# Kernel optimization log

Hardware: AMD Instinct MI355X
Metric: run time of the kernel (lower is better)

## Reference

```python
import jax, jax.numpy as jnp
import numpy as np

N_E, N_C, H = 100000, 50000, 256
D_E, D_C = 768, 1024
E_EE, E_EC, E_CE = 800000, 400000, 400000
EPS = 1e-12


def setup_inputs() -> dict:
    key = jax.random.key(0)
    ks = jax.random.split(key, 16)
    x_entity = jax.random.normal(ks[0], (N_E, D_E), jnp.float32)
    x_chunk = jax.random.normal(ks[1], (N_C, D_C), jnp.float32)
    # edge[0] = source indices, edge[1] = destination indices
    edge_ee = jnp.stack([jax.random.randint(ks[2], (E_EE,), 0, N_E),
                         jax.random.randint(ks[3], (E_EE,), 0, N_E)])
    edge_ec = jnp.stack([jax.random.randint(ks[4], (E_EC,), 0, N_E),
                         jax.random.randint(ks[5], (E_EC,), 0, N_C)])
    edge_ce = jnp.stack([jax.random.randint(ks[6], (E_CE,), 0, N_C),
                         jax.random.randint(ks[7], (E_CE,), 0, N_E)])
    # per-type projection weights (stored [in, out]; y = x @ W)
    P_e = jax.random.normal(ks[8], (D_E, H), jnp.float32) / np.sqrt(D_E).astype(np.float32)
    P_c = jax.random.normal(ks[9], (D_C, H), jnp.float32) / np.sqrt(D_C).astype(np.float32)
    s = np.float32(1.0 / np.sqrt(H))
    # SAGEConv params stacked over the 3 edge types: 0=e->e, 1=e->c, 2=c->e
    Wl1 = jax.random.normal(ks[10], (3, H, H), jnp.float32) * s
    bl1 = jnp.zeros((3, H), jnp.float32)
    Wr1 = jax.random.normal(ks[11], (3, H, H), jnp.float32) * s
    Wl2 = jax.random.normal(ks[12], (3, H, H), jnp.float32) * s
    bl2 = jnp.zeros((3, H), jnp.float32)
    Wr2 = jax.random.normal(ks[13], (3, H, H), jnp.float32) * s
    return {"x_entity": x_entity, "x_chunk": x_chunk,
            "edge_ee": edge_ee, "edge_ec": edge_ec, "edge_ce": edge_ce,
            "P_e": P_e, "P_c": P_c,
            "Wl1": Wl1, "bl1": bl1, "Wr1": Wr1,
            "Wl2": Wl2, "bl2": bl2, "Wr2": Wr2}


def _sage(x_src, x_dst, edge, Wl, bl, Wr, n_dst):
    # PyG SAGEConv: lin_l(mean of neighbor features) + lin_r(x_dst)
    msg = x_src[edge[0]]                                   # [E, H] gather
    agg = jax.ops.segment_sum(msg, edge[1], num_segments=n_dst)
    cnt = jax.ops.segment_sum(jnp.ones((edge.shape[1], 1), x_src.dtype),
                              edge[1], num_segments=n_dst)
    mean = agg / jnp.maximum(cnt, 1.0)                     # isolated nodes -> 0
    return mean @ Wl + bl + x_dst @ Wr


def _l2norm(v):
    # F.normalize(v, dim=1), eps=1e-12
    n = jnp.sqrt(jnp.sum(v * v, axis=1, keepdims=True))
    return v / jnp.maximum(n, EPS)


def reference(x_entity, x_chunk, edge_ee, edge_ec, edge_ce,
              P_e, P_c, Wl1, bl1, Wr1, Wl2, bl2, Wr2):
    # per-type projection (bias=False)
    h_e = x_entity @ P_e
    h_c = x_chunk @ P_c
    id_e, id_c = h_e, h_c
    # conv1: HeteroConv(aggr='sum') -> sum SAGE outputs per destination type
    o_e = (_sage(h_e, h_e, edge_ee, Wl1[0], bl1[0], Wr1[0], N_E)
           + _sage(h_c, h_e, edge_ce, Wl1[2], bl1[2], Wr1[2], N_E))
    o_c = _sage(h_e, h_c, edge_ec, Wl1[1], bl1[1], Wr1[1], N_C)
    # dropout(0.1) is identity in eval; relu then residual
    h_e = jax.nn.relu(o_e) + id_e
    h_c = jax.nn.relu(o_c) + id_c
    # conv2
    o_e = (_sage(h_e, h_e, edge_ee, Wl2[0], bl2[0], Wr2[0], N_E)
           + _sage(h_c, h_e, edge_ce, Wl2[2], bl2[2], Wr2[2], N_E))
    o_c = _sage(h_e, h_c, edge_ec, Wl2[1], bl2[1], Wr2[1], N_C)
    return _l2norm(o_e), _l2norm(o_c)
```

## Files before the change

kernel.cpp:

```cpp
#include <hip/hip_runtime.h>
#include <hip/hip_bf16.h>

#define N_E 100000
#define N_C 50000
#define H 256
#define D_E 768
#define D_C 1024
#define E_EE 800000
#define E_EC 400000
#define E_CE 400000
#define E_TOT (E_EE + E_CE + E_EC)

#define ME_PAD 100096
#define MC_PAD 50048

#define LDSZ 24576

typedef unsigned short u16;
typedef __attribute__((ext_vector_type(8))) short bf16x8;
typedef __attribute__((ext_vector_type(4))) float f32x4;

__device__ __forceinline__ float bf2f(u16 x) {
    unsigned u = ((unsigned)x) << 16;
    return __builtin_bit_cast(float, u);
}
__device__ __forceinline__ u16 f2bf(float f) {
    unsigned u = __builtin_bit_cast(unsigned, f);
    u = (u + 0x7fffu + ((u >> 16) & 1u)) >> 16;
    return (u16)u;
}

struct TransJobs {
    const float* a[12];
    const float* b[12];
    u16* dst[12];
    int K[12];
};

__global__ __launch_bounds__(1024) void transpose_all_k(TransJobs t) {
    int j = blockIdx.z;
    int K = t.K[j];
    int k0 = blockIdx.x * 32;
    if (k0 >= K) return;
    int n0 = blockIdx.y * 32;
    __shared__ float sm[32][33];
    int tx = threadIdx.x, ty = threadIdx.y;
    size_t idx = (size_t)(k0 + ty) * H + n0 + tx;
    float v = t.a[j][idx];
    if (t.b[j]) v += t.b[j][idx];
    sm[ty][tx] = v;
    __syncthreads();
    t.dst[j][(size_t)(n0 + ty) * K + k0 + tx] = f2bf(sm[tx][ty]);
}

__global__ __launch_bounds__(256) void hist3_k(const int* __restrict__ eeD,
                                               const int* __restrict__ ceD,
                                               const int* __restrict__ ecD,
                                               int* __restrict__ cnt) {
    int i = blockIdx.x * 256 + threadIdx.x;
    if (i >= E_TOT) return;
    if (i < E_EE) atomicAdd(&cnt[eeD[i]], 1);
    else if (i < E_EE + E_CE) atomicAdd(&cnt[N_E + ceD[i - E_EE]], 1);
    else atomicAdd(&cnt[2 * N_E + ecD[i - E_EE - E_CE]], 1);
}

#define SCAN_N (2 * N_E + N_C)
#define SCAN_NB ((SCAN_N + 1023) / 1024)

__global__ __launch_bounds__(1024) void scan_blk_k(const int* __restrict__ cnt,
                                                   int* __restrict__ part,
                                                   int* __restrict__ bsum) {
    __shared__ int sm[1024];
    int i = blockIdx.x * 1024 + threadIdx.x;
    int v = (i < SCAN_N) ? cnt[i] : 0;
    sm[threadIdx.x] = v;
    __syncthreads();
    for (int off = 1; off < 1024; off <<= 1) {
        int t = (threadIdx.x >= off) ? sm[threadIdx.x - off] : 0;
        __syncthreads();
        sm[threadIdx.x] += t;
        __syncthreads();
    }
    if (i < SCAN_N) part[i] = sm[threadIdx.x] - v;
    if (threadIdx.x == 1023) bsum[blockIdx.x] = sm[1023];
}

__global__ __launch_bounds__(1024) void scan_top_k(int* __restrict__ bsum) {
    __shared__ int sm[1024];
    int v = (threadIdx.x < SCAN_NB) ? bsum[threadIdx.x] : 0;
    sm[threadIdx.x] = v;
    __syncthreads();
    for (int off = 1; off < 1024; off <<= 1) {
        int t = (threadIdx.x >= off) ? sm[threadIdx.x - off] : 0;
        __syncthreads();
        sm[threadIdx.x] += t;
        __syncthreads();
    }
    if (threadIdx.x < SCAN_NB) bsum[threadIdx.x] = sm[threadIdx.x] - v;
}

__global__ __launch_bounds__(1024) void scan_out_k(const int* __restrict__ part,
                                                   const int* __restrict__ bsum,
                                                   int* __restrict__ eePtr,
                                                   int* __restrict__ cePtr,
                                                   int* __restrict__ ecPtr,
                                                   int* __restrict__ curAll) {
    int i = blockIdx.x * 1024 + threadIdx.x;
    if (i < SCAN_N) {
        int v = part[i] + bsum[blockIdx.x];
        int w;
        if (i < N_E) {
            w = v; eePtr[i] = w;
        } else if (i < 2 * N_E) {
            w = v - E_EE; cePtr[i - N_E] = w;
        } else {
            w = v - (E_EE + E_CE); ecPtr[i - 2 * N_E] = w;
        }
        curAll[i] = w;
    }
    if (i == 0) {
        eePtr[N_E] = E_EE;
        cePtr[N_E] = E_CE;
        ecPtr[N_C] = E_EC;
    }
}

__global__ __launch_bounds__(256) void reorder3_k(const int* __restrict__ eeS, const int* __restrict__ eeD,
                                                  const int* __restrict__ ceS, const int* __restrict__ ceD,
                                                  const int* __restrict__ ecS, const int* __restrict__ ecD,
                                                  int* __restrict__ curAll, int* __restrict__ srcAll) {
    int i = blockIdx.x * 256 + threadIdx.x;
    if (i >= E_TOT) return;
    if (i < E_EE) {
        int pos = atomicAdd(&curAll[eeD[i]], 1);
        srcAll[pos] = eeS[i];
    } else if (i < E_EE + E_CE) {
        int k = i - E_EE;
        int pos = atomicAdd(&curAll[N_E + ceD[k]], 1);
        srcAll[E_EE + pos] = ceS[k];
    } else {
        int k = i - E_EE - E_CE;
        int pos = atomicAdd(&curAll[2 * N_E + ecD[k]], 1);
        srcAll[E_EE + E_CE + pos] = ecS[k];
    }
}

struct GatherArgs {
    const u16* feat[3];
    const int* rowptr[3];
    const int* srcIdx[3];
    u16* outAgg[3];
    int nDst[3];
    int blkEnd[3];
};

__device__ __forceinline__ void acc8(float* a, uint4 v) {
    a[0] += __builtin_bit_cast(float, v.x << 16);
    a[1] += __builtin_bit_cast(float, v.x & 0xffff0000u);
    a[2] += __builtin_bit_cast(float, v.y << 16);
    a[3] += __builtin_bit_cast(float, v.y & 0xffff0000u);
    a[4] += __builtin_bit_cast(float, v.z << 16);
    a[5] += __builtin_bit_cast(float, v.z & 0xffff0000u);
    a[6] += __builtin_bit_cast(float, v.w << 16);
    a[7] += __builtin_bit_cast(float, v.w & 0xffff0000u);
}

__global__ __launch_bounds__(256) void gather3_k(GatherArgs a) {
    const int b = blockIdx.x;
    const int j = (b >= a.blkEnd[0]) + (b >= a.blkEnd[1]);
    const int b0 = j ? a.blkEnd[j - 1] : 0;
    const int r = (b - b0) * 4 + (threadIdx.x >> 6);
    const int lane = threadIdx.x & 63;
    const int half = lane >> 5;
    const int pos = lane & 31;

    float acc[8] = {};
    int deg = 0;
    if (r < a.nDst[j]) {
        const int* __restrict__ rp = a.rowptr[j];
        const int* __restrict__ si = a.srcIdx[j];
        const u16* __restrict__ ft = a.feat[j];
        int e0 = rp[r], e1 = rp[r + 1];
        deg = e1 - e0;
        int e = e0;
        for (; e + 7 < e1; e += 8) {
            int sA = si[e + half];
            int sB = si[e + 2 + half];
            int sC = si[e + 4 + half];
            int sD = si[e + 6 + half];
            uint4 vA = *(const uint4*)(ft + (size_t)sA * H + pos * 8);
            uint4 vB = *(const uint4*)(ft + (size_t)sB * H + pos * 8);
            uint4 vC = *(const uint4*)(ft + (size_t)sC * H + pos * 8);
            uint4 vD = *(const uint4*)(ft + (size_t)sD * H + pos * 8);
            acc8(acc, vA); acc8(acc, vB); acc8(acc, vC); acc8(acc, vD);
        }
        for (; e + 3 < e1; e += 4) {
            int sA = si[e + half];
            int sB = si[e + 2 + half];
            uint4 vA = *(const uint4*)(ft + (size_t)sA * H + pos * 8);
            uint4 vB = *(const uint4*)(ft + (size_t)sB * H + pos * 8);
            acc8(acc, vA); acc8(acc, vB);
        }
        for (; e + 1 < e1; e += 2) {
            int s = si[e + half];
            uint4 v = *(const uint4*)(ft + (size_t)s * H + pos * 8);
            acc8(acc, v);
        }
        if (e < e1 && half == 0) {
            int s = si[e];
            uint4 v = *(const uint4*)(ft + (size_t)s * H + pos * 8);
            acc8(acc, v);
        }
    }
#pragma unroll
    for (int k = 0; k < 8; ++k) acc[k] += __shfl_xor(acc[k], 32);

    if (half == 0) {
        float inv = deg > 0 ? 1.f / (float)deg : 0.f;
        uint4 o;
        o.x = (unsigned)f2bf(acc[0] * inv) | ((unsigned)f2bf(acc[1] * inv) << 16);
        o.y = (unsigned)f2bf(acc[2] * inv) | ((unsigned)f2bf(acc[3] * inv) << 16);
        o.z = (unsigned)f2bf(acc[4] * inv) | ((unsigned)f2bf(acc[5] * inv) << 16);
        o.w = (unsigned)f2bf(acc[6] * inv) | ((unsigned)f2bf(acc[7] * inv) << 16);
        *(uint4*)(a.outAgg[j] + (size_t)r * H + pos * 8) = o;
    }
}

struct GemmCfg {
    const u16* A[3];
    const u16* Wt[3];
    int nPairs;
    const float* bias1;
    const float* bias2;
    const u16* res;
    void* out;
    int Mvalid;
    int mode;
};
struct ConvArgs2 {
    GemmCfg c[2];
    int blkSplit;
};

__global__ __launch_bounds__(512, 4) void gemm_conv_k(ConvArgs2 gg) {
    const int which = blockIdx.x >= gg.blkSplit;
    const GemmCfg* __restrict__ g = which ? &gg.c[1] : &gg.c[0];
    const int row0 = (blockIdx.x - (which ? gg.blkSplit : 0)) * 128;

    __shared__ char lds[3][LDSZ];
    __shared__ float rowsq[128];
    const int tid = threadIdx.x;
    const int lane = tid & 63;
    const int wid = tid >> 6;
    const int wm = wid >> 2;
    const int wn = wid & 3;

    const int srow = tid >> 2;
    const int au = (tid & 3) ^ ((srow >> 1) & 3);
    const int ofsA = (row0 + srow) * H + au * 8;
    const int ofsB1 = srow * H + au * 8;
    const int brow2 = 128 + srow;
    const int bu2 = (tid & 3) ^ ((brow2 >> 1) & 3);
    const int ofsB2 = brow2 * H + bu2 * 8;

    int a_off[4], b_off[4];
#pragma unroll
    for (int mi = 0; mi < 4; ++mi) {
        int row = wm * 64 + mi * 16 + (lane & 15);
        int u = (lane >> 4) ^ ((row >> 1) & 3);
        a_off[mi] = row * 64 + u * 16;
    }
#pragma unroll
    for (int ni = 0; ni < 4; ++ni) {
        int row = wn * 64 + ni * 16 + (lane & 15);
        int u = (lane >> 4) ^ ((row >> 1) & 3);
        b_off[ni] = 8192 + row * 64 + u * 16;
    }

#define STAGE(p_, kk_, buf_)                                                                      \
    do {                                                                                          \
        const u16* A_ = g->A[p_];                                                                 \
        const u16* W_ = g->Wt[p_];                                                                \
        __builtin_amdgcn_global_load_lds(                                                         \
            (const __attribute__((address_space(1))) void*)(A_ + ofsA + (kk_)),                   \
            (__attribute__((address_space(3))) void*)((buf_) + wid * 1024), 16, 0, 0);            \
        __builtin_amdgcn_global_load_lds(                                                         \
            (const __attribute__((address_space(1))) void*)(W_ + ofsB1 + (kk_)),                  \
            (__attribute__((address_space(3))) void*)((buf_) + 8192 + wid * 1024), 16, 0, 0);     \
        __builtin_amdgcn_global_load_lds(                                                         \
            (const __attribute__((address_space(1))) void*)(W_ + ofsB2 + (kk_)),                  \
            (__attribute__((address_space(3))) void*)((buf_) + 16384 + wid * 1024), 16, 0, 0);    \
    } while (0)

    f32x4 acc[4][4] = {};
    const int T = g->nPairs * (H >> 5);

    char* bufC = lds[0];
    char* bufN = lds[1];
    char* bufS = lds[2];

    STAGE(0, 0, bufC);
    STAGE(0, 32, bufN);
    int pn = 0, kn = 64;
    if (kn == H) { kn = 0; pn = 1; }

    for (int s = 0; s < T; ++s) {
        if (s + 2 < T) {
            STAGE(pn, kn, bufS);
            kn += 32;
            if (kn == H) { kn = 0; ++pn; }
            asm volatile("s_waitcnt vmcnt(6)" ::: "memory");
        } else if (s + 1 < T) {
            asm volatile("s_waitcnt vmcnt(3)" ::: "memory");
        } else {
            asm volatile("s_waitcnt vmcnt(0)" ::: "memory");
        }
        __builtin_amdgcn_sched_barrier(0);
        __builtin_amdgcn_s_barrier();

        bf16x8 af[4], bfr[4];
#pragma unroll
        for (int mi = 0; mi < 4; ++mi)
            af[mi] = *reinterpret_cast<const bf16x8*>(bufC + a_off[mi]);
#pragma unroll
        for (int ni = 0; ni < 4; ++ni)
            bfr[ni] = *reinterpret_cast<const bf16x8*>(bufC + b_off[ni]);
#pragma unroll
        for (int mi = 0; mi < 4; ++mi)
#pragma unroll
            for (int ni = 0; ni < 4; ++ni)
                acc[mi][ni] = __builtin_amdgcn_mfma_f32_16x16x32_bf16(af[mi], bfr[ni],
                                                                      acc[mi][ni], 0, 0, 0);
        __builtin_amdgcn_sched_barrier(0);
        __builtin_amdgcn_s_barrier();
        char* t = bufC; bufC = bufN; bufN = bufS; bufS = t;
    }
#undef STAGE

    const int ccol = wn * 64 + (lane & 15);
    const int crow0 = row0 + wm * 64 + ((lane >> 4) << 2);
    float bv[4];
#pragma unroll
    for (int ni = 0; ni < 4; ++ni) {
        int c = ccol + ni * 16;
        float b = 0.f;
        if (g->bias1) b += g->bias1[c];
        if (g->bias2) b += g->bias2[c];
        bv[ni] = b;
    }

    if (g->mode == 1) {
#pragma unroll
        for (int ni = 0; ni < 4; ++ni) {
            int c = ccol + ni * 16;
#pragma unroll
            for (int mi = 0; mi < 4; ++mi) {
#pragma unroll
                for (int j = 0; j < 4; ++j) {
                    int r = crow0 + mi * 16 + j;
                    size_t idx = (size_t)r * H + c;
                    float v = fmaxf(acc[mi][ni][j] + bv[ni], 0.f) + bf2f(g->res[idx]);
                    ((u16*)g->out)[idx] = f2bf(v);
                }
            }
        }
    } else {
        if (tid < 128) rowsq[tid] = 0.f;
        __syncthreads();
#pragma unroll
        for (int mi = 0; mi < 4; ++mi) {
#pragma unroll
            for (int j = 0; j < 4; ++j) {
                float p = 0.f;
#pragma unroll
                for (int ni = 0; ni < 4; ++ni) {
                    float v = acc[mi][ni][j] + bv[ni];
                    p += v * v;
                }
                p += __shfl_xor(p, 1);
                p += __shfl_xor(p, 2);
                p += __shfl_xor(p, 4);
                p += __shfl_xor(p, 8);
                if ((lane & 15) == 0) {
                    int rl = wm * 64 + mi * 16 + ((lane >> 4) << 2) + j;
                    atomicAdd(&rowsq[rl], p);
                }
            }
        }
        __syncthreads();
#pragma unroll
        for (int mi = 0; mi < 4; ++mi) {
#pragma unroll
            for (int j = 0; j < 4; ++j) {
                int rl = wm * 64 + mi * 16 + ((lane >> 4) << 2) + j;
                int r = row0 + rl;
                if (r < g->Mvalid) {
                    float inv = 1.f / fmaxf(sqrtf(rowsq[rl]), 1e-12f);
#pragma unroll
                    for (int ni = 0; ni < 4; ++ni) {
                        int c = ccol + ni * 16;
                        float v = acc[mi][ni][j] + bv[ni];
                        ((float*)g->out)[(size_t)r * H + c] = v * inv;
                    }
                }
            }
        }
    }
}

struct ProjArgs2 {
    const float* A[2];
    const u16* Wt[2];
    int K[2];
    int M[2];
    u16* out[2];
    int blkSplit;
};

__global__ __launch_bounds__(512, 4) void gemm_proj_k(ProjArgs2 gg) {
    const int which = blockIdx.x >= gg.blkSplit;
    const int row0 = (blockIdx.x - (which ? gg.blkSplit : 0)) * 128;
    const float* __restrict__ Aptr = gg.A[which];
    const u16* __restrict__ Wt = gg.Wt[which];
    const int K = gg.K[which];
    const int M = gg.M[which];
    u16* __restrict__ outp = gg.out[which];

    __shared__ char lds[3][LDSZ];
    const int tid = threadIdx.x;
    const int lane = tid & 63;
    const int wid = tid >> 6;
    const int wm = wid >> 2;
    const int wn = wid & 3;

    const int srow = tid >> 2;
    const int cunit = tid & 3;
    const int aRow = min(row0 + srow, M - 1);
    const float* pA = Aptr + (size_t)aRow * K + cunit * 8;
    const int aDst = srow * 64 + (cunit ^ ((srow >> 1) & 3)) * 16;

    const int bu1 = cunit ^ ((srow >> 1) & 3);
    const int ofsB1 = srow * K + bu1 * 8;
    const int brow2 = 128 + srow;
    const int bu2 = cunit ^ ((brow2 >> 1) & 3);
    const int ofsB2 = brow2 * K + bu2 * 8;

    int a_off[4], b_off[4];
#pragma unroll
    for (int mi = 0; mi < 4; ++mi) {
        int row = wm * 64 + mi * 16 + (lane & 15);
        int u = (lane >> 4) ^ ((row >> 1) & 3);
        a_off[mi] = row * 64 + u * 16;
    }
#pragma unroll
    for (int ni = 0; ni < 4; ++ni) {
        int row = wn * 64 + ni * 16 + (lane & 15);
        int u = (lane >> 4) ^ ((row >> 1) & 3);
        b_off[ni] = 8192 + row * 64 + u * 16;
    }

#define BSTAGE(kk_, buf_)                                                                         \
    do {                                                                                          \
        __builtin_amdgcn_global_load_lds(                                                         \
            (const __attribute__((address_space(1))) void*)(Wt + ofsB1 + (kk_)),                  \
            (__attribute__((address_space(3))) void*)((buf_) + 8192 + wid * 1024), 16, 0, 0);     \
        __builtin_amdgcn_global_load_lds(                                                         \
            (const __attribute__((address_space(1))) void*)(Wt + ofsB2 + (kk_)),                  \
            (__attribute__((address_space(3))) void*)((buf_) + 16384 + wid * 1024), 16, 0, 0);    \
    } while (0)

    f32x4 acc[4][4] = {};
    const int T = K >> 5;

    char* bufC = lds[0];
    char* bufN = lds[1];
    char* bufS = lds[2];

    BSTAGE(0, bufC);
    float4 cA0 = *reinterpret_cast<const float4*>(pA);
    float4 cA1 = *reinterpret_cast<const float4*>(pA + 4);
    BSTAGE(32, bufN);
    float4 cB0 = *reinterpret_cast<const float4*>(pA + 32);
    float4 cB1 = *reinterpret_cast<const float4*>(pA + 36);

#define PITER(s_, c0_, c1_)                                                                       \
    do {                                                                                          \
        const int s = (s_);                                                                       \
        if (s + 2 < T) {                                                                          \
            BSTAGE((s + 2) * 32, bufS);                                                           \
            asm volatile("s_waitcnt vmcnt(6)" ::: "memory");                                      \
        } else if (s + 1 < T) {                                                                   \
            asm volatile("s_waitcnt vmcnt(4)" ::: "memory");                                      \
        } else {                                                                                  \
            asm volatile("s_waitcnt vmcnt(0)" ::: "memory");                                      \
        }                                                                                         \
        union { bf16x8 v; u16 e[8]; } pk;                                                         \
        pk.e[0] = f2bf(c0_.x); pk.e[1] = f2bf(c0_.y);                                             \
        pk.e[2] = f2bf(c0_.z); pk.e[3] = f2bf(c0_.w);                                             \
        pk.e[4] = f2bf(c1_.x); pk.e[5] = f2bf(c1_.y);                                             \
        pk.e[6] = f2bf(c1_.z); pk.e[7] = f2bf(c1_.w);                                             \
        *reinterpret_cast<bf16x8*>(bufC + aDst) = pk.v;                                           \
        if (s + 2 < T) {                                                                          \
            c0_ = *reinterpret_cast<const float4*>(pA + (s + 2) * 32);                            \
            c1_ = *reinterpret_cast<const float4*>(pA + (s + 2) * 32 + 4);                        \
        }                                                                                         \
        asm volatile("s_waitcnt lgkmcnt(0)" ::: "memory");                                        \
        __builtin_amdgcn_sched_barrier(0);                                                        \
        __builtin_amdgcn_s_barrier();                                                             \
        bf16x8 af[4], bfr[4];                                                                     \
        _Pragma("unroll")                                                                         \
        for (int mi = 0; mi < 4; ++mi)                                                            \
            af[mi] = *reinterpret_cast<const bf16x8*>(bufC + a_off[mi]);                          \
        _Pragma("unroll")                                                                         \
        for (int ni = 0; ni < 4; ++ni)                                                            \
            bfr[ni] = *reinterpret_cast<const bf16x8*>(bufC + b_off[ni]);                         \
        _Pragma("unroll")                                                                         \
        for (int mi = 0; mi < 4; ++mi)                                                            \
            _Pragma("unroll")                                                                     \
            for (int ni = 0; ni < 4; ++ni)                                                        \
                acc[mi][ni] = __builtin_amdgcn_mfma_f32_16x16x32_bf16(af[mi], bfr[ni],            \
                                                                      acc[mi][ni], 0, 0, 0);      \
        __builtin_amdgcn_sched_barrier(0);                                                        \
        __builtin_amdgcn_s_barrier();                                                             \
        char* t_ = bufC; bufC = bufN; bufN = bufS; bufS = t_;                                     \
    } while (0)

    for (int s2 = 0; s2 < T; s2 += 2) {
        PITER(s2, cA0, cA1);
        PITER(s2 + 1, cB0, cB1);
    }
#undef PITER
#undef BSTAGE

    const int ccol = wn * 64 + (lane & 15);
    const int crow0 = row0 + wm * 64 + ((lane >> 4) << 2);
#pragma unroll
    for (int ni = 0; ni < 4; ++ni) {
        int c = ccol + ni * 16;
#pragma unroll
        for (int mi = 0; mi < 4; ++mi) {
#pragma unroll
            for (int j = 0; j < 4; ++j) {
                int r = crow0 + mi * 16 + j;
                outp[(size_t)r * H + c] = f2bf(acc[mi][ni][j]);
            }
        }
    }
}

extern "C" void kernel_launch(void* const* d_in, const int* in_sizes, int n_in,
                              void* d_out, int out_size, void* d_ws, size_t ws_size,
                              hipStream_t stream) {
    const float* x_e = (const float*)d_in[0];
    const float* x_c = (const float*)d_in[1];
    const int* e_ee = (const int*)d_in[2];
    const int* e_ec = (const int*)d_in[3];
    const int* e_ce = (const int*)d_in[4];
    const float* P_e = (const float*)d_in[5];
    const float* P_c = (const float*)d_in[6];
    const float* Wl1 = (const float*)d_in[7];
    const float* bl1 = (const float*)d_in[8];
    const float* Wr1 = (const float*)d_in[9];
    const float* Wl2 = (const float*)d_in[10];
    const float* bl2 = (const float*)d_in[11];
    const float* Wr2 = (const float*)d_in[12];
    float* out = (float*)d_out;

    const size_t EHp = (size_t)ME_PAD * H;
    const size_t CHp = (size_t)MC_PAD * H;

    u16* us = (u16*)d_ws;
    u16* he0 = us;   us += EHp;
    u16* he1 = us;   us += EHp;
    u16* aggE1 = us; us += EHp;
    u16* aggE2 = us; us += EHp;
    u16* hc0 = us;   us += CHp;
    u16* hc1 = us;   us += CHp;
    u16* aggC = us;  us += CHp;
    u16* PeT = us;   us += H * D_E;
    u16* PcT = us;   us += H * D_C;
    u16* WlT1 = us;  us += 3 * H * H;
    u16* WrT1_1 = us; us += H * H;
    u16* WrT1s = us;  us += H * H;
    u16* WlT2 = us;  us += 3 * H * H;
    u16* WrT2_1 = us; us += H * H;
    u16* WrT2s = us;  us += H * H;

    int* ip = (int*)us;
    int* eePtr = ip;  ip += N_E + 1;
    int* cePtr = ip;  ip += N_E + 1;
    int* ecPtr = ip;  ip += N_C + 1;
    int* curAll = ip; ip += SCAN_N;
    int* srcAll = ip; ip += E_TOT;
    int* cntAll = ip; ip += SCAN_N;
    int* part = ip;   ip += SCAN_N;
    int* bsum = ip;   ip += SCAN_NB + 1;

    const int WHH = H * H;

    hipMemsetAsync(cntAll, 0, (size_t)SCAN_N * sizeof(int), stream);
    hist3_k<<<(E_TOT + 255) / 256, 256, 0, stream>>>(e_ee + E_EE, e_ce + E_CE, e_ec + E_EC, cntAll);
    scan_blk_k<<<SCAN_NB, 1024, 0, stream>>>(cntAll, part, bsum);
    scan_top_k<<<1, 1024, 0, stream>>>(bsum);
    scan_out_k<<<SCAN_NB, 1024, 0, stream>>>(part, bsum, eePtr, cePtr, ecPtr, curAll);
    reorder3_k<<<(E_TOT + 255) / 256, 256, 0, stream>>>(e_ee, e_ee + E_EE, e_ce, e_ce + E_CE,
                                                        e_ec, e_ec + E_EC, curAll, srcAll);
    const int* eeSrc = srcAll;
    const int* ceSrc = srcAll + E_EE;
    const int* ecSrc = srcAll + E_EE + E_CE;

    {
        TransJobs t{};
        int n = 0;
        auto add = [&](const float* a, const float* b, u16* d, int K) {
            t.a[n] = a; t.b[n] = b; t.dst[n] = d; t.K[n] = K; ++n;
        };
        add(P_e, nullptr, PeT, D_E);
        add(P_c, nullptr, PcT, D_C);
        for (int p = 0; p < 3; ++p) add(Wl1 + p * WHH, nullptr, WlT1 + p * WHH, H);
        for (int p = 0; p < 3; ++p) add(Wl2 + p * WHH, nullptr, WlT2 + p * WHH, H);
        add(Wr1 + 1 * WHH, nullptr, WrT1_1, H);
        add(Wr2 + 1 * WHH, nullptr, WrT2_1, H);
        add(Wr1 + 0 * WHH, Wr1 + 2 * WHH, WrT1s, H);
        add(Wr2 + 0 * WHH, Wr2 + 2 * WHH, WrT2s, H);
        transpose_all_k<<<dim3(D_C / 32, H / 32, 12), dim3(32, 32), 0, stream>>>(t);
    }

    const int gridE = ME_PAD / 128, gridC = MC_PAD / 128;

    {
        ProjArgs2 g{};
        g.A[0] = x_e; g.Wt[0] = PeT; g.K[0] = D_E; g.M[0] = N_E; g.out[0] = he0;
        g.A[1] = x_c; g.Wt[1] = PcT; g.K[1] = D_C; g.M[1] = N_C; g.out[1] = hc0;
        g.blkSplit = gridE;
        gemm_proj_k<<<gridE + gridC, 512, 0, stream>>>(g);
    }

    const int gBlkE = ME_PAD / 4, gBlkC = MC_PAD / 4;
    const int gTotal = 2 * gBlkE + gBlkC;

    {
        GatherArgs a{};
        a.feat[0] = he0; a.rowptr[0] = eePtr; a.srcIdx[0] = eeSrc; a.outAgg[0] = aggE1; a.nDst[0] = N_E;
        a.feat[1] = hc0; a.rowptr[1] = cePtr; a.srcIdx[1] = ceSrc; a.outAgg[1] = aggE2; a.nDst[1] = N_E;
        a.feat[2] = he0; a.rowptr[2] = ecPtr; a.srcIdx[2] = ecSrc; a.outAgg[2] = aggC;  a.nDst[2] = N_C;
        a.blkEnd[0] = gBlkE; a.blkEnd[1] = 2 * gBlkE; a.blkEnd[2] = gTotal;
        gather3_k<<<gTotal, 256, 0, stream>>>(a);
    }
    {
        ConvArgs2 g{};
        g.c[0].A[0] = aggE1; g.c[0].Wt[0] = WlT1 + 0 * WHH;
        g.c[0].A[1] = aggE2; g.c[0].Wt[1] = WlT1 + 2 * WHH;
        g.c[0].A[2] = he0;   g.c[0].Wt[2] = WrT1s;
        g.c[0].nPairs = 3;
        g.c[0].bias1 = bl1 + 0 * H; g.c[0].bias2 = bl1 + 2 * H;
        g.c[0].res = he0; g.c[0].out = he1; g.c[0].mode = 1;
        g.c[1].A[0] = aggC; g.c[1].Wt[0] = WlT1 + 1 * WHH;
        g.c[1].A[1] = hc0;  g.c[1].Wt[1] = WrT1_1;
        g.c[1].nPairs = 2;
        g.c[1].bias1 = bl1 + 1 * H;
        g.c[1].res = hc0; g.c[1].out = hc1; g.c[1].mode = 1;
        g.blkSplit = gridE;
        gemm_conv_k<<<gridE + gridC, 512, 0, stream>>>(g);
    }

    {
        GatherArgs a{};
        a.feat[0] = he1; a.rowptr[0] = eePtr; a.srcIdx[0] = eeSrc; a.outAgg[0] = aggE1; a.nDst[0] = N_E;
        a.feat[1] = hc1; a.rowptr[1] = cePtr; a.srcIdx[1] = ceSrc; a.outAgg[1] = aggE2; a.nDst[1] = N_E;
        a.feat[2] = he1; a.rowptr[2] = ecPtr; a.srcIdx[2] = ecSrc; a.outAgg[2] = aggC;  a.nDst[2] = N_C;
        a.blkEnd[0] = gBlkE; a.blkEnd[1] = 2 * gBlkE; a.blkEnd[2] = gTotal;
        gather3_k<<<gTotal, 256, 0, stream>>>(a);
    }
    {
        ConvArgs2 g{};
        g.c[0].A[0] = aggE1; g.c[0].Wt[0] = WlT2 + 0 * WHH;
        g.c[0].A[1] = aggE2; g.c[0].Wt[1] = WlT2 + 2 * WHH;
        g.c[0].A[2] = he1;   g.c[0].Wt[2] = WrT2s;
        g.c[0].nPairs = 3;
        g.c[0].bias1 = bl2 + 0 * H; g.c[0].bias2 = bl2 + 2 * H;
        g.c[0].out = out; g.c[0].Mvalid = N_E; g.c[0].mode = 2;
        g.c[1].A[0] = aggC; g.c[1].Wt[0] = WlT2 + 1 * WHH;
        g.c[1].A[1] = hc1;  g.c[1].Wt[1] = WrT2_1;
        g.c[1].nPairs = 2;
        g.c[1].bias1 = bl2 + 1 * H;
        g.c[1].out = out + (size_t)N_E * H; g.c[1].Mvalid = N_C; g.c[1].mode = 2;
        g.blkSplit = gridE;
        gemm_conv_k<<<gridE + gridC, 512, 0, stream>>>(g);
    }
}
```

Before: 869.0 us.

## Enlarge conv GEMM tile to 256 rows with 64-deep K double-buffered pipeline

Replaces the 128-row conv GEMM kernel with a 256-row tile variant in which each wave computes 8x4 MFMA tiles. It uses 64-wide K steps split into four staged load groups over two 64KB LDS buffers, with s_setprio around the MFMA blocks. The goal is better weight reuse and fewer barriers per FLOP. In exchange it needs much more LDS and registers (launch bounds 1), so occupancy drops, and MC_PAD grows so the chunk rows divide evenly into 256-row tiles.

```diff
diff --git a/kernel.cpp b/kernel.cpp
--- a/kernel.cpp
+++ b/kernel.cpp
@@ -12,7 +12,7 @@
 #define E_TOT (E_EE + E_CE + E_EC)
 
 #define ME_PAD 100096
-#define MC_PAD 50048
+#define MC_PAD 50176
 
 #define LDSZ 24576
 
@@ -242,103 +242,171 @@
     int blkSplit;
 };
 
-__global__ __launch_bounds__(512, 4) void gemm_conv_k(ConvArgs2 gg) {
+__global__ __launch_bounds__(512, 1) void gemm_conv8_k(ConvArgs2 gg) {
     const int which = blockIdx.x >= gg.blkSplit;
     const GemmCfg* __restrict__ g = which ? &gg.c[1] : &gg.c[0];
-    const int row0 = (blockIdx.x - (which ? gg.blkSplit : 0)) * 128;
-
-    __shared__ char lds[3][LDSZ];
-    __shared__ float rowsq[128];
+    const int row0 = (blockIdx.x - (which ? gg.blkSplit : 0)) * 256;
+
+    __shared__ char lds[2][65536];
+    __shared__ float rowsq[256];
     const int tid = threadIdx.x;
     const int lane = tid & 63;
     const int wid = tid >> 6;
     const int wm = wid >> 2;
     const int wn = wid & 3;
 
-    const int srow = tid >> 2;
-    const int au = (tid & 3) ^ ((srow >> 1) & 3);
-    const int ofsA = (row0 + srow) * H + au * 8;
-    const int ofsB1 = srow * H + au * 8;
-    const int brow2 = 128 + srow;
-    const int bu2 = (tid & 3) ^ ((brow2 >> 1) & 3);
-    const int ofsB2 = brow2 * H + bu2 * 8;
-
-    int a_off[4], b_off[4];
-#pragma unroll
-    for (int mi = 0; mi < 4; ++mi) {
-        int row = wm * 64 + mi * 16 + (lane & 15);
-        int u = (lane >> 4) ^ ((row >> 1) & 3);
-        a_off[mi] = row * 64 + u * 16;
+    const int rowL0 = wid * 16 + (lane >> 2);
+    const int rowL1 = 128 + rowL0;
+    const int u0 = (lane & 3) ^ ((rowL0 >> 1) & 3);
+    const int u1 = (lane & 3) ^ ((rowL1 >> 1) & 3);
+    const int ofsA0 = (row0 + rowL0) * H + u0 * 8;
+    const int ofsA1 = (row0 + rowL1) * H + u1 * 8;
+    const int ofsB0 = rowL0 * H + u0 * 8;
+    const int ofsB1 = rowL1 * H + u1 * 8;
+
+    int ao[8], bo[4];
+#pragma unroll
+    for (int mi = 0; mi < 8; ++mi) {
+        int r = wm * 128 + mi * 16 + (lane & 15);
+        int u = (lane >> 4) ^ ((r >> 1) & 3);
+        ao[mi] = r * 64 + u * 16;
     }
 #pragma unroll
     for (int ni = 0; ni < 4; ++ni) {
-        int row = wn * 64 + ni * 16 + (lane & 15);
-        int u = (lane >> 4) ^ ((row >> 1) & 3);
-        b_off[ni] = 8192 + row * 64 + u * 16;
-    }
-
-#define STAGE(p_, kk_, buf_)                                                                      \
-    do {                                                                                          \
-        const u16* A_ = g->A[p_];                                                                 \
-        const u16* W_ = g->Wt[p_];                                                                \
-        __builtin_amdgcn_global_load_lds(                                                         \
-            (const __attribute__((address_space(1))) void*)(A_ + ofsA + (kk_)),                   \
-            (__attribute__((address_space(3))) void*)((buf_) + wid * 1024), 16, 0, 0);            \
-        __builtin_amdgcn_global_load_lds(                                                         \
-            (const __attribute__((address_space(1))) void*)(W_ + ofsB1 + (kk_)),                  \
-            (__attribute__((address_space(3))) void*)((buf_) + 8192 + wid * 1024), 16, 0, 0);     \
-        __builtin_amdgcn_global_load_lds(                                                         \
-            (const __attribute__((address_space(1))) void*)(W_ + ofsB2 + (kk_)),                  \
-            (__attribute__((address_space(3))) void*)((buf_) + 16384 + wid * 1024), 16, 0, 0);    \
+        int r = wn * 64 + ni * 16 + (lane & 15);
+        int u = (lane >> 4) ^ ((r >> 1) & 3);
+        bo[ni] = 16384 + r * 64 + u * 16;
+    }
+
+#define STG(st_)                                                                                   \
+    do {                                                                                           \
+        const u16* src_ = ((st_) & 1) ? nW : nA;                                                   \
+        const int e0_ = (((st_) & 1) ? ofsB0 : ofsA0) + kn + ((st_) >> 1) * 32;                    \
+        const int e1_ = (((st_) & 1) ? ofsB1 : ofsA1) + kn + ((st_) >> 1) * 32;                    \
+        __builtin_amdgcn_global_load_lds(                                                          \
+            (const __attribute__((address_space(1))) void*)(src_ + e0_),                           \
+            (__attribute__((address_space(3))) void*)(bufN + (st_) * 16384 + wid * 1024), 16, 0, 0); \
+        __builtin_amdgcn_global_load_lds(                                                          \
+            (const __attribute__((address_space(1))) void*)(src_ + e1_),                           \
+            (__attribute__((address_space(3))) void*)(bufN + (st_) * 16384 + 8192 + wid * 1024),   \
+            16, 0, 0);                                                                             \
     } while (0)
 
-    f32x4 acc[4][4] = {};
-    const int T = g->nPairs * (H >> 5);
-
-    char* bufC = lds[0];
-    char* bufN = lds[1];
-    char* bufS = lds[2];
-
-    STAGE(0, 0, bufC);
-    STAGE(0, 32, bufN);
-    int pn = 0, kn = 64;
-    if (kn == H) { kn = 0; pn = 1; }
+    f32x4 acc[8][4] = {};
+    const int T = g->nPairs * (H / 64);
+
+    int pn = 0, kn = 0;
+    {
+        const u16* nA = g->A[0];
+        const u16* nW = g->Wt[0];
+        char* bufN = lds[0];
+        STG(0); STG(1); STG(2); STG(3);
+    }
+    kn = 64;
 
     for (int s = 0; s < T; ++s) {
-        if (s + 2 < T) {
-            STAGE(pn, kn, bufS);
-            kn += 32;
-            if (kn == H) { kn = 0; ++pn; }
+        char* bufC = lds[s & 1];
+        char* bufN = lds[(s + 1) & 1];
+        const bool more = (s + 1 < T);
+        const u16* nA = g->A[more ? pn : 0];
+        const u16* nW = g->Wt[more ? pn : 0];
+        bf16x8 bfr[4];
+
+        if (more) {
+            STG(0);
             asm volatile("s_waitcnt vmcnt(6)" ::: "memory");
-        } else if (s + 1 < T) {
-            asm volatile("s_waitcnt vmcnt(3)" ::: "memory");
+        } else {
+            asm volatile("s_waitcnt vmcnt(4)" ::: "memory");
+        }
+        __builtin_amdgcn_sched_barrier(0);
+        __builtin_amdgcn_s_barrier();
+        {
+#pragma unroll
+            for (int ni = 0; ni < 4; ++ni) bfr[ni] = *(const bf16x8*)(bufC + bo[ni]);
+            bf16x8 af[4];
+#pragma unroll
+            for (int i = 0; i < 4; ++i) af[i] = *(const bf16x8*)(bufC + ao[i]);
+            __builtin_amdgcn_s_setprio(1);
+#pragma unroll
+            for (int i = 0; i < 4; ++i)
+#pragma unroll
+                for (int ni = 0; ni < 4; ++ni)
+                    acc[i][ni] = __builtin_amdgcn_mfma_f32_16x16x32_bf16(af[i], bfr[ni],
+                                                                         acc[i][ni], 0, 0, 0);
+            __builtin_amdgcn_s_setprio(0);
+        }
+        __builtin_amdgcn_sched_barrier(0);
+        __builtin_amdgcn_s_barrier();
+
+        if (more) STG(1);
+        {
+            bf16x8 af[4];
+#pragma unroll
+            for (int i = 0; i < 4; ++i) af[i] = *(const bf16x8*)(bufC + ao[4 + i]);
+            __builtin_amdgcn_s_setprio(1);
+#pragma unroll
+            for (int i = 0; i < 4; ++i)
+#pragma unroll
+                for (int ni = 0; ni < 4; ++ni)
+                    acc[4 + i][ni] = __builtin_amdgcn_mfma_f32_16x16x32_bf16(af[i], bfr[ni],
+                                                                             acc[4 + i][ni], 0, 0, 0);
+            __builtin_amdgcn_s_setprio(0);
+        }
+        __builtin_amdgcn_sched_barrier(0);
+        __builtin_amdgcn_s_barrier();
+
+        if (more) {
+            STG(2);
+            asm volatile("s_waitcnt vmcnt(6)" ::: "memory");
         } else {
             asm volatile("s_waitcnt vmcnt(0)" ::: "memory");
         }
         __builtin_amdgcn_sched_barrier(0);
         __builtin_amdgcn_s_barrier();
-
-        bf16x8 af[4], bfr[4];
-#pragma unroll
-        for (int mi = 0; mi < 4; ++mi)
-            af[mi] = *reinterpret_cast<const bf16x8*>(bufC + a_off[mi]);
-#pragma unroll
-        for (int ni = 0; ni < 4; ++ni)
-            bfr[ni] = *reinterpret_cast<const bf16x8*>(bufC + b_off[ni]);
-#pragma unroll
-        for (int mi = 0; mi < 4; ++mi)
-#pragma unroll
-            for (int ni = 0; ni < 4; ++ni)
-                acc[mi][ni] = __builtin_amdgcn_mfma_f32_16x16x32_bf16(af[mi], bfr[ni],
-                                                                      acc[mi][ni], 0, 0, 0);
+        {
+#pragma unroll
+            for (int ni = 0; ni < 4; ++ni) bfr[ni] = *(const bf16x8*)(bufC + 32768 + bo[ni]);
+            bf16x8 af[4];
+#pragma unroll
+            for (int i = 0; i < 4; ++i) af[i] = *(const bf16x8*)(bufC + 32768 + ao[i]);
+            __builtin_amdgcn_s_setprio(1);
+#pragma unroll
+            for (int i = 0; i < 4; ++i)
+#pragma unroll
+                for (int ni = 0; ni < 4; ++ni)
+                    acc[i][ni] = __builtin_amdgcn_mfma_f32_16x16x32_bf16(af[i], bfr[ni],
+                                                                         acc[i][ni], 0, 0, 0);
+            __builtin_amdgcn_s_setprio(0);
+        }
         __builtin_amdgcn_sched_barrier(0);
         __builtin_amdgcn_s_barrier();
-        char* t = bufC; bufC = bufN; bufN = bufS; bufS = t;
-    }
-#undef STAGE
+
+        if (more) STG(3);
+        {
+            bf16x8 af[4];
+#pragma unroll
+            for (int i = 0; i < 4; ++i) af[i] = *(const bf16x8*)(bufC + 32768 + ao[4 + i]);
+            __builtin_amdgcn_s_setprio(1);
+#pragma unroll
+            for (int i = 0; i < 4; ++i)
+#pragma unroll
+                for (int ni = 0; ni < 4; ++ni)
+                    acc[4 + i][ni] = __builtin_amdgcn_mfma_f32_16x16x32_bf16(af[i], bfr[ni],
+                                                                             acc[4 + i][ni], 0, 0, 0);
+            __builtin_amdgcn_s_setprio(0);
+        }
+        __builtin_amdgcn_sched_barrier(0);
+        __builtin_amdgcn_s_barrier();
+
+        if (more) {
+            kn += 64;
+            if (kn == H) { kn = 0; ++pn; }
+        }
+    }
+#undef STG
 
     const int ccol = wn * 64 + (lane & 15);
-    const int crow0 = row0 + wm * 64 + ((lane >> 4) << 2);
+    const int crow0 = row0 + wm * 128 + ((lane >> 4) << 2);
     float bv[4];
 #pragma unroll
     for (int ni = 0; ni < 4; ++ni) {
@@ -354,7 +422,7 @@
         for (int ni = 0; ni < 4; ++ni) {
             int c = ccol + ni * 16;
 #pragma unroll
-            for (int mi = 0; mi < 4; ++mi) {
+            for (int mi = 0; mi < 8; ++mi) {
 #pragma unroll
                 for (int j = 0; j < 4; ++j) {
                     int r = crow0 + mi * 16 + j;
@@ -365,10 +433,10 @@
             }
         }
     } else {
-        if (tid < 128) rowsq[tid] = 0.f;
+        if (tid < 256) rowsq[tid] = 0.f;
         __syncthreads();
 #pragma unroll
-        for (int mi = 0; mi < 4; ++mi) {
+        for (int mi = 0; mi < 8; ++mi) {
 #pragma unroll
             for (int j = 0; j < 4; ++j) {
                 float p = 0.f;
@@ -382,17 +450,17 @@
                 p += __shfl_xor(p, 4);
                 p += __shfl_xor(p, 8);
                 if ((lane & 15) == 0) {
-                    int rl = wm * 64 + mi * 16 + ((lane >> 4) << 2) + j;
+                    int rl = wm * 128 + mi * 16 + ((lane >> 4) << 2) + j;
                     atomicAdd(&rowsq[rl], p);
                 }
             }
         }
         __syncthreads();
 #pragma unroll
-        for (int mi = 0; mi < 4; ++mi) {
+        for (int mi = 0; mi < 8; ++mi) {
 #pragma unroll
             for (int j = 0; j < 4; ++j) {
-                int rl = wm * 64 + mi * 16 + ((lane >> 4) << 2) + j;
+                int rl = wm * 128 + mi * 16 + ((lane >> 4) << 2) + j;
                 int r = row0 + rl;
                 if (r < g->Mvalid) {
                     float inv = 1.f / fmaxf(sqrtf(rowsq[rl]), 1e-12f);
@@ -638,6 +706,7 @@
 
     const int gBlkE = ME_PAD / 4, gBlkC = MC_PAD / 4;
     const int gTotal = 2 * gBlkE + gBlkC;
+    const int g8E = ME_PAD / 256, g8C = MC_PAD / 256;
 
     {
         GatherArgs a{};
@@ -654,14 +723,14 @@
         g.c[0].A[2] = he0;   g.c[0].Wt[2] = WrT1s;
         g.c[0].nPairs = 3;
         g.c[0].bias1 = bl1 + 0 * H; g.c[0].bias2 = bl1 + 2 * H;
-        g.c[0].res = he0; g.c[0].out = he1; g.c[0].mode = 1;
+        g.c[0].res = he0; g.c[0].out = he1; g.c[0].Mvalid = N_E; g.c[0].mode = 1;
         g.c[1].A[0] = aggC; g.c[1].Wt[0] = WlT1 + 1 * WHH;
         g.c[1].A[1] = hc0;  g.c[1].Wt[1] = WrT1_1;
         g.c[1].nPairs = 2;
         g.c[1].bias1 = bl1 + 1 * H;
-        g.c[1].res = hc0; g.c[1].out = hc1; g.c[1].mode = 1;
-        g.blkSplit = gridE;
-        gemm_conv_k<<<gridE + gridC, 512, 0, stream>>>(g);
+        g.c[1].res = hc0; g.c[1].out = hc1; g.c[1].Mvalid = N_C; g.c[1].mode = 1;
+        g.blkSplit = g8E;
+        gemm_conv8_k<<<g8E + g8C, 512, 0, stream>>>(g);
     }
 
     {
@@ -685,7 +754,7 @@
         g.c[1].nPairs = 2;
         g.c[1].bias1 = bl2 + 1 * H;
         g.c[1].out = out + (size_t)N_E * H; g.c[1].Mvalid = N_C; g.c[1].mode = 2;
-        g.blkSplit = gridE;
-        gemm_conv_k<<<gridE + gridC, 512, 0, stream>>>(g);
-    }
-}
+        g.blkSplit = g8E;
+        gemm_conv8_k<<<g8E + g8C, 512, 0, stream>>>(g);
+    }
+}
```

Result: slower. 959.7 us (+10.4%).
